# Kernel tuning notes

Measured on AMD Instinct MI355X. Metric: run time of the kernel, lower is better.

The kernel has to match this reference:

```python
import jax, jax.numpy as jnp
import numpy as np

B, H, L, N = 16, 256, 4096, 64  # N = d_state//2 retained complex-conjugate modes (S4D)
EPS = 1e-5


def setup_inputs() -> dict:
    key = jax.random.key(0)
    ks = jax.random.split(key, 6)
    x = jax.random.normal(ks[0], (B, H, L), dtype=jnp.float32)
    # dt log-uniform in [1e-3, 1e-1] per channel (standard S4 init)
    log_dt = (jax.random.uniform(ks[1], (H,), dtype=jnp.float32)
              * (np.log(0.1) - np.log(0.001)) + np.log(0.001))
    # S4D-Lin init: A_n = -1/2 + i*pi*n
    A_re = -0.5 * jnp.ones((H, N), dtype=jnp.float32)
    A_im = jnp.pi * jnp.broadcast_to(jnp.arange(N, dtype=jnp.float32), (H, N))
    # bidirectional -> 2 channel groups of C
    C_re = jax.random.normal(ks[2], (2, H, N), dtype=jnp.float32)
    C_im = jax.random.normal(ks[3], (2, H, N), dtype=jnp.float32)
    D = jax.random.normal(ks[4], (H,), dtype=jnp.float32)
    ln_w = jnp.ones((H,), dtype=jnp.float32)
    ln_b = jnp.zeros((H,), dtype=jnp.float32)
    W_out = jax.random.normal(ks[5], (H, H), dtype=jnp.float32) / np.sqrt(H)
    b_out = jnp.zeros((H,), dtype=jnp.float32)
    return {"x": x, "log_dt": log_dt, "A_re": A_re, "A_im": A_im,
            "C_re": C_re, "C_im": C_im, "D": D,
            "ln_w": ln_w, "ln_b": ln_b, "W_out": W_out, "b_out": b_out}


def _s4_forward(x, log_dt, A_re, A_im, C_re, C_im, D, ln_w, ln_b, W_out, b_out):
    # LayerNorm over channel dim (x.transpose -> LN(d_model) -> transpose back)
    mu = jnp.mean(x, axis=1, keepdims=True)
    var = jnp.mean((x - mu) ** 2, axis=1, keepdims=True)
    z = (x - mu) * jax.lax.rsqrt(var + EPS) * ln_w[None, :, None] + ln_b[None, :, None]

    # --- S4D kernel via Vandermonde (ZOH-style discretization) ---
    A = A_re + 1j * A_im                         # (H, N)
    C = C_re + 1j * C_im                         # (2, H, N)
    dt = jnp.exp(log_dt)[:, None]                # (H, 1)
    dtA = dt * A                                 # (H, N)
    C_t = C * (jnp.exp(dtA) - 1.0) / A           # (2, H, N)
    t = jnp.arange(L, dtype=jnp.float32)
    V = jnp.exp(dtA[:, :, None] * t)             # (H, N, L) Vandermonde
    K = 2.0 * jnp.real(jnp.einsum('dhn,hnl->dhl', C_t, V))  # (2, H, L)

    # bidirectional: forward kernel padded right, backward kernel flipped, padded left
    k = jnp.pad(K[0], ((0, 0), (0, L))) + jnp.pad(K[1][:, ::-1], ((0, 0), (L, 0)))

    # FFT convolution over length 2L
    Uf = jnp.fft.rfft(z, n=2 * L)                # (B, H, L+1)
    Kf = jnp.fft.rfft(k, n=2 * L)                # (H, L+1)
    y = jnp.fft.irfft(Uf * Kf[None], n=2 * L)[..., :L]

    y = y + D[None, :, None] * z                 # skip D*u
    y = jax.nn.gelu(y)                           # S4 default activation
    # transposed position-wise output linear (postact=None -> plain Linear)
    y = jnp.einsum('oh,bhl->bol', W_out, y) + b_out[None, :, None]
    return x + y                                  # residual


def reference(x, log_dt, A_re, A_im, C_re, C_im, D, ln_w, ln_b, W_out, b_out):
    return _s4_forward(x, log_dt, A_re, A_im, C_re, C_im, D, ln_w, ln_b, W_out, b_out)
```

## Files before the change

kernel.cpp:

```cpp
#include <hip/hip_runtime.h>
#include <math.h>

#define B_ 16
#define H_ 256
#define L_ 4096
#define N_ 64
#define HN (H_*N_)
#define HL (H_*L_)
#define BHL (B_*H_*L_)
#define SPAD 64

#define WVT_OFS 0
#define TM_OFS  8192
#define E2T_OFS 12288
#define MATS_PER 20480

typedef short bf16x8 __attribute__((ext_vector_type(8)));
typedef float f32x4  __attribute__((ext_vector_type(4)));

__device__ __forceinline__ unsigned int pk2(float a, float b) {
    return ((__float_as_uint(a) + 0x8000u) >> 16) |
           ((__float_as_uint(b) + 0x8000u) & 0xffff0000u);
}
__device__ __forceinline__ unsigned short bfr(float a) {
    return (unsigned short)((__float_as_uint(a) + 0x8000u) >> 16);
}
__device__ __forceinline__ float ubf(unsigned short u) {
    return __uint_as_float(((unsigned int)u) << 16);
}

__global__ void __launch_bounds__(64) mats_kernel(const float* __restrict__ log_dt,
                                                  const float* __restrict__ A_re,
                                                  const float* __restrict__ A_im,
                                                  const float* __restrict__ C_re,
                                                  const float* __restrict__ C_im,
                                                  unsigned short* __restrict__ mats,
                                                  float2* __restrict__ Wc) {
    int hd = blockIdx.x;
    int h = hd >> 1, d = hd & 1;
    int m = threadIdx.x;
    __shared__ float2 pws[65 * 64];
    __shared__ float2 c2s[64];
    __shared__ float  Karr[64];

    int i = h * 64 + m;
    float dt = expf(log_dt[h]);
    float Are = A_re[i], Aim = A_im[i];
    float dr = dt * Are, di = dt * Aim;
    float er = expf(dr);
    float wr = er * cosf(di), wi = er * sinf(di);
    float em1r = wr - 1.0f, em1i = wi;
    float inv = 1.0f / (Are * Are + Aim * Aim);
    float qr = (em1r * Are + em1i * Aim) * inv;
    float qi = (em1i * Are - em1r * Aim) * inv;
    float Cr = C_re[d * HN + i], Ci = C_im[d * HN + i];
    float2 c2;
    c2.x = 2.0f * (Cr * qr - Ci * qi);
    c2.y = 2.0f * (Cr * qi + Ci * qr);
    c2s[m] = c2;
    float pr = 1.0f, pi = 0.0f;
    for (int k = 0; k < 64; ++k) {
        float2 p; p.x = pr; p.y = pi;
        pws[k * 64 + ((m + k) & 63)] = p;
        float t = pr * wr - pi * wi;
        pi = pr * wi + pi * wr;
        pr = t;
    }
    {
        float2 p; p.x = pr; p.y = pi;
        pws[64 * 64 + ((m + 64) & 63)] = p;
        Wc[hd * 64 + m] = p;
    }
    __syncthreads();
    {
        float kk = 0.f;
        for (int mm = 0; mm < 64; ++mm) {
            float2 c = c2s[mm];
            float2 pw = pws[m * 64 + ((mm + m) & 63)];
            kk += c.x * pw.x - c.y * pw.y;
        }
        Karr[m] = kk;
    }
    __syncthreads();
    unsigned short* mb = mats + (size_t)hd * MATS_PER;
    for (int i2 = 0; i2 < 32; ++i2) {
        int e0 = 2 * i2, e1 = e0 + 1;
        int k0 = d ? e0 : 63 - e0;
        int k1 = d ? e1 : 63 - e1;
        float2 p0 = pws[k0 * 64 + ((m + k0) & 63)];
        float2 p1 = pws[k1 * 64 + ((m + k1) & 63)];
        *(unsigned int*)(mb + WVT_OFS + (2 * m) * 64 + e0)     = pk2(p0.x, p1.x);
        *(unsigned int*)(mb + WVT_OFS + (2 * m + 1) * 64 + e0) = pk2(p0.y, p1.y);
    }
    for (int i2 = 0; i2 < 32; ++i2) {
        int e0 = 2 * i2, e1 = e0 + 1;
        float v0, v1;
        if (d == 0) {
            v0 = (e0 <= m) ? Karr[m - e0] : 0.f;
            v1 = (e1 <= m) ? Karr[m - e1] : 0.f;
        } else {
            v0 = (e0 > m) ? Karr[e0 - m - 1] : 0.f;
            v1 = (e1 > m) ? Karr[e1 - m - 1] : 0.f;
        }
        *(unsigned int*)(mb + TM_OFS + m * 64 + e0) = pk2(v0, v1);
    }
    {
        int kp = d ? (63 - m) : (m + 1);
        for (int mm = 0; mm < 64; ++mm) {
            float2 c = c2s[mm];
            float2 pw = pws[kp * 64 + ((mm + kp) & 63)];
            float vr = c.x * pw.x - c.y * pw.y;
            float vi = -(c.x * pw.y + c.y * pw.x);
            *(unsigned int*)(mb + E2T_OFS + m * 128 + 2 * mm) = pk2(vr, vi);
        }
    }
}

__global__ void __launch_bounds__(256) wbf_kernel(const float* __restrict__ W,
                                                  unsigned short* __restrict__ Wbf) {
    int i = (blockIdx.x * 256 + threadIdx.x) * 4;
    float4 v = *(const float4*)(W + i);
    uint2 u;
    u.x = pk2(v.x, v.y);
    u.y = pk2(v.z, v.w);
    *(uint2*)(Wbf + i) = u;
}

__global__ void __launch_bounds__(256) ln_kernel(const float* __restrict__ x,
                                                 const float* __restrict__ lnw,
                                                 const float* __restrict__ lnb,
                                                 unsigned short* __restrict__ zb) {
    int b  = blockIdx.y;
    int l0 = blockIdx.x * 256;
    int t  = threadIdx.x;
    int hq = t >> 6, lo = t & 63;
    int l  = l0 + lo * 4;
    __shared__ float4 r1[4][64];
    __shared__ float4 r2[4][64];
    __shared__ float4 muS[64];
    __shared__ float4 rsS[64];
    const float* xb = x + (size_t)b * HL;
    float4 s1 = {0.f,0.f,0.f,0.f}, s2 = {0.f,0.f,0.f,0.f};
    #pragma unroll 4
    for (int hh = 0; hh < 64; ++hh) {
        int h = hq * 64 + hh;
        float4 v = *(const float4*)(xb + (size_t)h * L_ + l);
        s1.x += v.x; s1.y += v.y; s1.z += v.z; s1.w += v.w;
        s2.x += v.x*v.x; s2.y += v.y*v.y; s2.z += v.z*v.z; s2.w += v.w*v.w;
    }
    r1[hq][lo] = s1; r2[hq][lo] = s2;
    __syncthreads();
    if (t < 64) {
        float4 S1 = r1[0][t], S2 = r2[0][t];
        #pragma unroll
        for (int q = 1; q < 4; ++q) {
            float4 a = r1[q][t], c = r2[q][t];
            S1.x += a.x; S1.y += a.y; S1.z += a.z; S1.w += a.w;
            S2.x += c.x; S2.y += c.y; S2.z += c.z; S2.w += c.w;
        }
        const float invH = 1.0f / 256.0f;
        float4 mu, rs;
        mu.x = S1.x*invH; mu.y = S1.y*invH; mu.z = S1.z*invH; mu.w = S1.w*invH;
        rs.x = rsqrtf(S2.x*invH - mu.x*mu.x + 1e-5f);
        rs.y = rsqrtf(S2.y*invH - mu.y*mu.y + 1e-5f);
        rs.z = rsqrtf(S2.z*invH - mu.z*mu.z + 1e-5f);
        rs.w = rsqrtf(S2.w*invH - mu.w*mu.w + 1e-5f);
        muS[t] = mu; rsS[t] = rs;
    }
    __syncthreads();
    float4 mu = muS[lo], rs = rsS[lo];
    #pragma unroll 4
    for (int hh = 0; hh < 64; ++hh) {
        int h = hq * 64 + hh;
        float w = lnw[h], bb = lnb[h];
        float4 v = *(const float4*)(xb + (size_t)h * L_ + l);
        float4 zz;
        zz.x = (v.x - mu.x) * rs.x * w + bb;
        zz.y = (v.y - mu.y) * rs.y * w + bb;
        zz.z = (v.z - mu.z) * rs.z * w + bb;
        zz.w = (v.w - mu.w) * rs.w * w + bb;
        uint2 u;
        u.x = pk2(zz.x, zz.y);
        u.y = pk2(zz.z, zz.w);
        *(uint2*)(zb + (size_t)b * HL + (size_t)h * L_ + l) = u;
    }
}

#define MFMA16(a,b,c) __builtin_amdgcn_mfma_f32_16x16x32_bf16((a),(b),(c),0,0,0)
#define SU_BASE 8192

__global__ void __launch_bounds__(128, 3) ssm_kernel(const unsigned short* __restrict__ zb,
                                                     const unsigned short* __restrict__ mats,
                                                     const float2* __restrict__ Wc,
                                                     const float* __restrict__ D,
                                                     unsigned short* __restrict__ y2) {
    int bhd = blockIdx.x;
    int d  = bhd & 1;
    int bh = bhd >> 1;
    int h  = bh & (H_ - 1);
    int t  = threadIdx.x;
    int w  = t >> 6, l = t & 63;
    int p  = w;

    __shared__ __align__(16) char smem[24576];

    const unsigned short* mb = mats + (size_t)(h * 2 + d) * MATS_PER;

    {
        const char* zrow = (const char*)(zb + (size_t)bh * L_);
        #pragma unroll
        for (int k = 0; k < 4; ++k) {
            int row = w * 32 + k * 8 + (l >> 3);
            int chunk = (l & 7) ^ (row & 7);
            const char* src = zrow + row * 128 + chunk * 16;
            __builtin_amdgcn_global_load_lds(
                (const __attribute__((address_space(1))) unsigned int*)src,
                (__attribute__((address_space(3))) unsigned int*)(smem + w * 4096 + k * 1024),
                16, 0, 0);
        }
    }
    __syncthreads();

    bf16x8 za[4][2];
    int arow = l & 15;
    int koff = (l >> 4) * 8;
    #pragma unroll
    for (int cb = 0; cb < 4; ++cb) {
        int row = cb * 16 + arow;
        unsigned int sw = (row & 7) << 4;
        #pragma unroll
        for (int kb = 0; kb < 2; ++kb) {
            unsigned int byte = (unsigned)(row * 128 + (kb * 32 + koff) * 2) ^ sw;
            za[cb][kb] = *(bf16x8*)(smem + byte);
        }
    }

    char* sUd = smem + SU_BASE;
    #pragma unroll
    for (int mcb = 0; mcb < 4; ++mcb) {
        int mcblk = p * 4 + mcb;
        const unsigned short* wv = mb + WVT_OFS + (mcblk * 16 + arow) * 64 + koff;
        bf16x8 b0 = *(const bf16x8*)(wv);
        bf16x8 b1 = *(const bf16x8*)(wv + 32);
        #pragma unroll
        for (int cb = 0; cb < 4; ++cb) {
            f32x4 acc = {0.f, 0.f, 0.f, 0.f};
            acc = MFMA16(za[cb][0], b0, acc);
            acc = MFMA16(za[cb][1], b1, acc);
            int mc = mcblk * 16 + arow;
            #pragma unroll
            for (int rr = 0; rr < 4; ++rr) {
                int c = cb * 16 + (l >> 4) * 4 + rr;
                unsigned int byte = ((unsigned)(c * 256 + mc * 2)) ^ ((c & 7) << 4);
                *(unsigned short*)(sUd + byte) = bfr(acc[rr]);
            }
        }
    }
    __syncthreads();

    if (p == 0) {
        float2 w64 = Wc[(h * 2 + d) * 64 + l];
        float sr = 0.f, si = 0.f;
        if (d == 0) {
            for (int c = 0; c < 64; ++c) {
                unsigned int byte = ((unsigned)(c * 256 + l * 4)) ^ ((c & 7) << 4);
                unsigned int uu = *(unsigned int*)(sUd + byte);
                float ur = __uint_as_float(uu << 16);
                float ui = __uint_as_float(uu & 0xffff0000u);
                *(unsigned int*)(sUd + byte) = pk2(sr, si);
                float nsr = fmaf(w64.x, sr, fmaf(-w64.y, si, ur));
                float nsi = fmaf(w64.x, si, fmaf(w64.y, sr, ui));
                sr = nsr; si = nsi;
            }
        } else {
            for (int c = 63; c >= 0; --c) {
                unsigned int byte = ((unsigned)(c * 256 + l * 4)) ^ ((c & 7) << 4);
                unsigned int uu = *(unsigned int*)(sUd + byte);
                float ur = __uint_as_float(uu << 16);
                float ui = __uint_as_float(uu & 0xffff0000u);
                *(unsigned int*)(sUd + byte) = pk2(sr, si);
                float nsr = fmaf(w64.x, sr, fmaf(-w64.y, si, ur));
                float nsi = fmaf(w64.x, si, fmaf(w64.y, sr, ui));
                sr = nsr; si = nsi;
            }
        }
    }
    __syncthreads();

    f32x4 yacc[2][4];
    #pragma unroll
    for (int jb = 0; jb < 2; ++jb) {
        int jblk = p * 2 + jb;
        const unsigned short* tm = mb + TM_OFS + (jblk * 16 + arow) * 64 + koff;
        bf16x8 tb0 = *(const bf16x8*)(tm);
        bf16x8 tb1 = *(const bf16x8*)(tm + 32);
        const unsigned short* et = mb + E2T_OFS + (jblk * 16 + arow) * 128 + koff;
        bf16x8 eb0 = *(const bf16x8*)(et);
        bf16x8 eb1 = *(const bf16x8*)(et + 32);
        bf16x8 eb2 = *(const bf16x8*)(et + 64);
        bf16x8 eb3 = *(const bf16x8*)(et + 96);
        #pragma unroll
        for (int cb = 0; cb < 4; ++cb) {
            f32x4 acc = {0.f, 0.f, 0.f, 0.f};
            acc = MFMA16(za[cb][0], tb0, acc);
            acc = MFMA16(za[cb][1], tb1, acc);
            int row = cb * 16 + arow;
            unsigned int sw = (row & 7) << 4;
            bf16x8 sa0 = *(bf16x8*)(sUd + (((unsigned)(row * 256 + (0 * 32 + koff) * 2)) ^ sw));
            bf16x8 sa1 = *(bf16x8*)(sUd + (((unsigned)(row * 256 + (1 * 32 + koff) * 2)) ^ sw));
            bf16x8 sa2 = *(bf16x8*)(sUd + (((unsigned)(row * 256 + (2 * 32 + koff) * 2)) ^ sw));
            bf16x8 sa3 = *(bf16x8*)(sUd + (((unsigned)(row * 256 + (3 * 32 + koff) * 2)) ^ sw));
            acc = MFMA16(sa0, eb0, acc);
            acc = MFMA16(sa1, eb1, acc);
            acc = MFMA16(sa2, eb2, acc);
            acc = MFMA16(sa3, eb3, acc);
            yacc[jb][cb] = acc;
        }
    }
    __syncthreads();

    {
        float dv = D[h];
        #pragma unroll
        for (int jb = 0; jb < 2; ++jb) {
            int j = (p * 2 + jb) * 16 + arow;
            #pragma unroll
            for (int cb = 0; cb < 4; ++cb) {
                #pragma unroll
                for (int rr = 0; rr < 4; ++rr) {
                    int c = cb * 16 + (l >> 4) * 4 + rr;
                    unsigned int byte = ((unsigned)(c * 128 + j * 2)) ^ ((c & 7) << 4);
                    float val = yacc[jb][cb][rr];
                    if (d == 0) val += dv * ubf(*(unsigned short*)(smem + byte));
                    *(unsigned short*)(smem + byte) = bfr(val);
                }
            }
        }
    }
    __syncthreads();
    {
        int row = t >> 1, halfq = t & 1;
        unsigned int rsw = (row & 7) << 4;
        char* go = (char*)(y2 + ((size_t)bh * 2 + d) * L_);
        #pragma unroll
        for (int j = 0; j < 4; ++j) {
            unsigned int off = (unsigned)(row * 128 + halfq * 64 + j * 16);
            uint4 a = *(const uint4*)(smem + (off ^ rsw));
            *(uint4*)(go + off) = a;
        }
    }
}

__global__ void __launch_bounds__(256, 3) outproj_kernel(
        const unsigned short* __restrict__ y2,
        const unsigned short* __restrict__ Wbf,
        const float* __restrict__ x,
        const float* __restrict__ bias,
        float* __restrict__ out) {
    int b  = blockIdx.z;
    int o0 = blockIdx.y * 128;
    int l0 = blockIdx.x * 128;
    int t  = threadIdx.x;
    int w  = t >> 6, lane = t & 63;
    int wr = w >> 1, wc = w & 1;
    int l15 = lane & 15, q = lane >> 4;

    __shared__ __align__(16) char lds[34816];
    unsigned short* At = (unsigned short*)lds;
    unsigned short* Bt = (unsigned short*)(lds + 16384);

    f32x4 acc[4][4];
    #pragma unroll
    for (int i = 0; i < 4; ++i)
        #pragma unroll
        for (int j = 0; j < 4; ++j) acc[i][j] = (f32x4){0.f, 0.f, 0.f, 0.f};

    const unsigned short* Wb0 = Wbf + (size_t)o0 * 256;
    unsigned int swz = (unsigned)(l15 & 7) << 4;

    int h_loc = t >> 2, lq = t & 3;

    for (int kt = 0; kt < 4; ++kt) {
        int k0 = kt * 64;
        {
            const unsigned short* yb0 =
                y2 + (((size_t)b * H_ + k0 + h_loc) * 2) * L_ + l0 + lq * 32;
            uint4 f[4], g[4];
            #pragma unroll
            for (int j = 0; j < 4; ++j) f[j] = *(const uint4*)(yb0 + j * 8);
            #pragma unroll
            for (int j = 0; j < 4; ++j) g[j] = *(const uint4*)(yb0 + L_ + j * 8);
            #pragma unroll
            for (int j = 0; j < 4; ++j) {
                #pragma unroll
                for (int e = 0; e < 8; ++e) {
                    int l_loc = lq * 32 + j * 8 + e;
                    float y = ubf(((const unsigned short*)&f[j])[e]) +
                              ubf(((const unsigned short*)&g[j])[e]);
                    float inner = 0.7978845608028654f * (y + 0.044715f * y * y * y);
                    float en = __expf(-2.0f * inner);
                    float gv = y * __builtin_amdgcn_rcpf(1.0f + en);
                    *(unsigned short*)((char*)At +
                        (((unsigned)(l_loc * 128 + h_loc * 2)) ^ ((l_loc & 7) << 4))) = bfr(gv);
                }
            }
        }
        #pragma unroll
        for (int s = 0; s < 4; ++s) {
            int id = (w * 4 + s) * 64 + lane;
            int row = id >> 3, ch = id & 7;
            int chl = ch ^ (row & 7);
            uint4 vb = *(const uint4*)(Wb0 + (size_t)row * 256 + k0 + chl * 8);
            *(uint4*)(Bt + id * 8) = vb;
        }
        __syncthreads();
        #pragma unroll
        for (int kk = 0; kk < 2; ++kk) {
            bf16x8 af[4], bfr_[4];
            #pragma unroll
            for (int rb = 0; rb < 4; ++rb) {
                int li = wr * 64 + rb * 16 + l15;
                af[rb] = *(const bf16x8*)((char*)At + li * 128 + (((kk * 64 + q * 16)) ^ swz));
                int oi = wc * 64 + rb * 16 + l15;
                bfr_[rb] = *(const bf16x8*)((char*)Bt + oi * 128 + (((kk * 64 + q * 16)) ^ swz));
            }
            #pragma unroll
            for (int rb = 0; rb < 4; ++rb)
                #pragma unroll
                for (int cb = 0; cb < 4; ++cb)
                    acc[rb][cb] = MFMA16(af[rb], bfr_[cb], acc[rb][cb]);
        }
        __syncthreads();
    }

    float* Eb = (float*)lds;
    for (int pp = 0; pp < 2; ++pp) {
        if (wc == pp) {
            #pragma unroll
            for (int cb = 0; cb < 4; ++cb) {
                int o_loc = cb * 16 + l15;
                unsigned int esw = (unsigned)(o_loc & 7) << 4;
                #pragma unroll
                for (int rb = 0; rb < 4; ++rb) {
                    int colbase = wr * 64 + rb * 16 + q * 4;
                    #pragma unroll
                    for (int r = 0; r < 4; ++r) {
                        int col = colbase + r;
                        *(float*)((char*)Eb + o_loc * 528 + (((unsigned)(col * 4)) ^ esw)) =
                            acc[rb][cb][r];
                    }
                }
            }
        }
        __syncthreads();
        int o_loc = t >> 2, lseg = t & 3;
        int o = o0 + pp * 64 + o_loc;
        float bo = bias[o];
        unsigned int esw = (unsigned)(o_loc & 7) << 4;
        size_t off = ((size_t)b * H_ + o) * L_ + l0 + lseg * 32;
        const float* xr = x + off;
        float* orow = out + off;
        #pragma unroll
        for (int j = 0; j < 8; ++j) {
            float4 e = *(const float4*)((char*)Eb + o_loc * 528 +
                                        (((unsigned)(lseg * 128 + j * 16)) ^ esw));
            float4 xv = *(const float4*)(xr + j * 4);
            float4 ov;
            ov.x = xv.x + bo + e.x;
            ov.y = xv.y + bo + e.y;
            ov.z = xv.z + bo + e.z;
            ov.w = xv.w + bo + e.w;
            *(float4*)(orow + j * 4) = ov;
        }
        __syncthreads();
    }
}

extern "C" void kernel_launch(void* const* d_in, const int* in_sizes, int n_in,
                              void* d_out, int out_size, void* d_ws, size_t ws_size,
                              hipStream_t stream) {
    const float* x      = (const float*)d_in[0];
    const float* log_dt = (const float*)d_in[1];
    const float* A_re   = (const float*)d_in[2];
    const float* A_im   = (const float*)d_in[3];
    const float* C_re   = (const float*)d_in[4];
    const float* C_im   = (const float*)d_in[5];
    const float* D      = (const float*)d_in[6];
    const float* lnw    = (const float*)d_in[7];
    const float* lnb    = (const float*)d_in[8];
    const float* W      = (const float*)d_in[9];
    const float* bout   = (const float*)d_in[10];
    float* out = (float*)d_out;

    unsigned short* zb   = (unsigned short*)d_ws;
    unsigned short* y2   = zb + (size_t)BHL + SPAD;
    unsigned short* mats = y2 + 2 * (size_t)BHL + SPAD;
    float2* Wc = (float2*)(mats + 512 * (size_t)MATS_PER);
    unsigned short* Wbf = (unsigned short*)(Wc + 512 * 64);

    mats_kernel<<<512, 64, 0, stream>>>(log_dt, A_re, A_im, C_re, C_im, mats, Wc);
    wbf_kernel<<<64, 256, 0, stream>>>(W, Wbf);
    ln_kernel<<<dim3(L_ / 256, B_), 256, 0, stream>>>(x, lnw, lnb, zb);
    ssm_kernel<<<B_ * H_ * 2, 128, 0, stream>>>(zb, mats, Wc, D, y2);
    outproj_kernel<<<dim3(L_ / 128, H_ / 128, B_), 256, 0, stream>>>(y2, Wbf, x, bout, out);
}
```

Before: 189.6 us.

## Split chunk-state scan across both waves and read residual x as bf16

The sequential 64-step inter-chunk state recurrence in ssm_kernel, previously run by one wave, is split so each wave scans 32 chunks. The second half then gets a correction that propagates the mid-point state with powers of the decay factor, shortening the serial critical path. Separately, ln_kernel now also writes a bf16 copy of x, and outproj reads that copy for the residual add to halve its residual read traffic. The extra bf16 write in ln_kernel adds traffic that partly offsets the saving. The residual term loses precision by being rounded to bf16.

```diff
diff --git a/kernel.cpp b/kernel.cpp
--- a/kernel.cpp
+++ b/kernel.cpp
@@ -129,7 +129,8 @@
 __global__ void __launch_bounds__(256) ln_kernel(const float* __restrict__ x,
                                                  const float* __restrict__ lnw,
                                                  const float* __restrict__ lnb,
-                                                 unsigned short* __restrict__ zb) {
+                                                 unsigned short* __restrict__ zb,
+                                                 unsigned short* __restrict__ xbf) {
     int b  = blockIdx.y;
     int l0 = blockIdx.x * 256;
     int t  = threadIdx.x;
@@ -183,11 +184,16 @@
         u.x = pk2(zz.x, zz.y);
         u.y = pk2(zz.z, zz.w);
         *(uint2*)(zb + (size_t)b * HL + (size_t)h * L_ + l) = u;
+        uint2 ux;
+        ux.x = pk2(v.x, v.y);
+        ux.y = pk2(v.z, v.w);
+        *(uint2*)(xbf + (size_t)b * HL + (size_t)h * L_ + l) = ux;
     }
 }
 
 #define MFMA16(a,b,c) __builtin_amdgcn_mfma_f32_16x16x32_bf16((a),(b),(c),0,0,0)
 #define SU_BASE 8192
+#define SMID_BASE 24576
 
 __global__ void __launch_bounds__(128, 3) ssm_kernel(const unsigned short* __restrict__ zb,
                                                      const unsigned short* __restrict__ mats,
@@ -202,7 +208,7 @@
     int w  = t >> 6, l = t & 63;
     int p  = w;
 
-    __shared__ __align__(16) char smem[24576];
+    __shared__ __align__(16) char smem[25088];
 
     const unsigned short* mb = mats + (size_t)(h * 2 + d) * MATS_PER;
 
@@ -258,31 +264,43 @@
     }
     __syncthreads();
 
-    if (p == 0) {
-        float2 w64 = Wc[(h * 2 + d) * 64 + l];
+    float2 w64 = Wc[(h * 2 + d) * 64 + l];
+    float2* smid = (float2*)(smem + SMID_BASE);
+    {
         float sr = 0.f, si = 0.f;
-        if (d == 0) {
-            for (int c = 0; c < 64; ++c) {
-                unsigned int byte = ((unsigned)(c * 256 + l * 4)) ^ ((c & 7) << 4);
-                unsigned int uu = *(unsigned int*)(sUd + byte);
-                float ur = __uint_as_float(uu << 16);
-                float ui = __uint_as_float(uu & 0xffff0000u);
-                *(unsigned int*)(sUd + byte) = pk2(sr, si);
-                float nsr = fmaf(w64.x, sr, fmaf(-w64.y, si, ur));
-                float nsi = fmaf(w64.x, si, fmaf(w64.y, sr, ui));
-                sr = nsr; si = nsi;
-            }
-        } else {
-            for (int c = 63; c >= 0; --c) {
-                unsigned int byte = ((unsigned)(c * 256 + l * 4)) ^ ((c & 7) << 4);
-                unsigned int uu = *(unsigned int*)(sUd + byte);
-                float ur = __uint_as_float(uu << 16);
-                float ui = __uint_as_float(uu & 0xffff0000u);
-                *(unsigned int*)(sUd + byte) = pk2(sr, si);
-                float nsr = fmaf(w64.x, sr, fmaf(-w64.y, si, ur));
-                float nsi = fmaf(w64.x, si, fmaf(w64.y, sr, ui));
-                sr = nsr; si = nsi;
-            }
+        int cbase = (d == 0) ? (p ? 32 : 0) : (p ? 31 : 63);
+        int cstep = (d == 0) ? 1 : -1;
+        for (int k = 0; k < 32; ++k) {
+            int c = cbase + cstep * k;
+            unsigned int byte = ((unsigned)(c * 256 + l * 4)) ^ ((c & 7) << 4);
+            unsigned int uu = *(unsigned int*)(sUd + byte);
+            float ur = __uint_as_float(uu << 16);
+            float ui = __uint_as_float(uu & 0xffff0000u);
+            *(unsigned int*)(sUd + byte) = pk2(sr, si);
+            float nsr = fmaf(w64.x, sr, fmaf(-w64.y, si, ur));
+            float nsi = fmaf(w64.x, si, fmaf(w64.y, sr, ui));
+            sr = nsr; si = nsi;
+        }
+        if (p == 0) { float2 sm; sm.x = sr; sm.y = si; smid[l] = sm; }
+    }
+    __syncthreads();
+    if (p == 1) {
+        float2 sm = smid[l];
+        float pr2 = 1.f, pi2 = 0.f;
+        int cbase = (d == 0) ? 32 : 31;
+        int cstep = (d == 0) ? 1 : -1;
+        for (int k = 0; k < 32; ++k) {
+            int c = cbase + cstep * k;
+            unsigned int byte = ((unsigned)(c * 256 + l * 4)) ^ ((c & 7) << 4);
+            unsigned int uu = *(unsigned int*)(sUd + byte);
+            float tr_ = __uint_as_float(uu << 16);
+            float ti_ = __uint_as_float(uu & 0xffff0000u);
+            float cr_ = fmaf(pr2, sm.x, -pi2 * sm.y);
+            float ci_ = fmaf(pr2, sm.y,  pi2 * sm.x);
+            *(unsigned int*)(sUd + byte) = pk2(tr_ + cr_, ti_ + ci_);
+            float npr = pr2 * w64.x - pi2 * w64.y;
+            float npi = pr2 * w64.y + pi2 * w64.x;
+            pr2 = npr; pi2 = npi;
         }
     }
     __syncthreads();
@@ -354,7 +372,7 @@
 __global__ void __launch_bounds__(256, 3) outproj_kernel(
         const unsigned short* __restrict__ y2,
         const unsigned short* __restrict__ Wbf,
-        const float* __restrict__ x,
+        const unsigned short* __restrict__ xbf,
         const float* __restrict__ bias,
         float* __restrict__ out) {
     int b  = blockIdx.z;
@@ -458,18 +476,18 @@
         float bo = bias[o];
         unsigned int esw = (unsigned)(o_loc & 7) << 4;
         size_t off = ((size_t)b * H_ + o) * L_ + l0 + lseg * 32;
-        const float* xr = x + off;
+        const unsigned short* xr = xbf + off;
         float* orow = out + off;
         #pragma unroll
         for (int j = 0; j < 8; ++j) {
             float4 e = *(const float4*)((char*)Eb + o_loc * 528 +
                                         (((unsigned)(lseg * 128 + j * 16)) ^ esw));
-            float4 xv = *(const float4*)(xr + j * 4);
+            uint2 xv2 = *(const uint2*)(xr + j * 4);
             float4 ov;
-            ov.x = xv.x + bo + e.x;
-            ov.y = xv.y + bo + e.y;
-            ov.z = xv.z + bo + e.z;
-            ov.w = xv.w + bo + e.w;
+            ov.x = ubf((unsigned short)(xv2.x & 0xffffu))  + bo + e.x;
+            ov.y = ubf((unsigned short)(xv2.x >> 16))      + bo + e.y;
+            ov.z = ubf((unsigned short)(xv2.y & 0xffffu))  + bo + e.z;
+            ov.w = ubf((unsigned short)(xv2.y >> 16))      + bo + e.w;
             *(float4*)(orow + j * 4) = ov;
         }
         __syncthreads();
@@ -494,13 +512,14 @@
 
     unsigned short* zb   = (unsigned short*)d_ws;
     unsigned short* y2   = zb + (size_t)BHL + SPAD;
-    unsigned short* mats = y2 + 2 * (size_t)BHL + SPAD;
+    unsigned short* xbf  = y2 + 2 * (size_t)BHL + SPAD;
+    unsigned short* mats = xbf + (size_t)BHL + SPAD;
     float2* Wc = (float2*)(mats + 512 * (size_t)MATS_PER);
     unsigned short* Wbf = (unsigned short*)(Wc + 512 * 64);
 
     mats_kernel<<<512, 64, 0, stream>>>(log_dt, A_re, A_im, C_re, C_im, mats, Wc);
     wbf_kernel<<<64, 256, 0, stream>>>(W, Wbf);
-    ln_kernel<<<dim3(L_ / 256, B_), 256, 0, stream>>>(x, lnw, lnb, zb);
+    ln_kernel<<<dim3(L_ / 256, B_), 256, 0, stream>>>(x, lnw, lnb, zb, xbf);
     ssm_kernel<<<B_ * H_ * 2, 128, 0, stream>>>(zb, mats, Wc, D, y2);
-    outproj_kernel<<<dim3(L_ / 128, H_ / 128, B_), 256, 0, stream>>>(y2, Wbf, x, bout, out);
-}
+    outproj_kernel<<<dim3(L_ / 128, H_ / 128, B_), 256, 0, stream>>>(y2, Wbf, xbf, bout, out);
+}
```

Result: no change. 193.1 us (+1.8%).
